# Kernel optimization log

Hardware: AMD Instinct MI355X
Metric: run time of the kernel (lower is better)

Reference implementation:

```python
import jax, jax.numpy as jnp
import numpy as np

B, N, S, C, H = 16, 64, 4096, 768, 8
HD = C // H
SCALE = HD ** -0.5
ASSIGN_EPS = 1.0


def hard_softmax(logits, axis):
    # softmax over `axis`, then straight-through one-hot argmax along `axis`
    y_soft = jax.nn.softmax(logits, axis=axis)
    idx = jnp.argmax(y_soft, axis=axis, keepdims=True)
    n = logits.shape[axis]
    shape = [1] * logits.ndim
    shape[axis] = n
    iota = jnp.arange(n).reshape(shape)
    y_hard = (iota == idx).astype(logits.dtype)
    return y_hard - jax.lax.stop_gradient(y_soft) + y_soft


def setup_inputs() -> dict:
    key = jax.random.key(0)
    ks = jax.random.split(key, 7)
    w = lambda k, shp: (jax.random.normal(k, shp, dtype=jnp.float32) * 0.02)
    return {
        'query': jax.random.normal(ks[0], (B, N, C), dtype=jnp.float32),
        'key_in': jax.random.normal(ks[1], (B, S, C), dtype=jnp.float32),
        'Wq': w(ks[2], (C, C)),
        'Wk': w(ks[3], (C, C)),
        'Wv': w(ks[4], (C, C)),
        'Wo': w(ks[5], (C, C)),
        'bo': jnp.zeros((C,), dtype=jnp.float32),
    }


def reference(query, key_in, Wq, Wk, Wv, Wo, bo):
    # linear projections (torch Linear: x @ W.T), split heads -> b h n d
    q = jnp.einsum('bnc,dc->bnd', query, Wq).reshape(B, N, H, HD).transpose(0, 2, 1, 3)
    k = jnp.einsum('bsc,dc->bsd', key_in, Wk).reshape(B, S, H, HD).transpose(0, 2, 1, 3)
    v = jnp.einsum('bsc,dc->bsd', key_in, Wv).reshape(B, S, H, HD).transpose(0, 2, 1, 3)
    raw_attn = jnp.einsum('bhnd,bhsd->bhns', q, k) * SCALE      # [B,H,N,S]
    attn = hard_softmax(raw_attn, axis=-2)                       # hard assign over groups N
    attn = attn / (attn.sum(axis=-1, keepdims=True) + ASSIGN_EPS)  # renorm over tokens S
    out = jnp.einsum('bhns,bhsd->bhnd', attn, v)                 # [B,H,N,HD]
    out = out.transpose(0, 2, 1, 3).reshape(B, N, C)
    out = jnp.einsum('bnc,dc->bnd', out, Wo) + bo
    return out
```

## Files before the change

### kernel.cpp

```cpp
#include <hip/hip_runtime.h>

#define BB 16
#define NN 64
#define SS 4096
#define CC 768
#define HH 8
#define HD 96

typedef __attribute__((ext_vector_type(8))) short bf16x8;
typedef __attribute__((ext_vector_type(4))) float f32x4;
typedef __attribute__((ext_vector_type(8))) unsigned short u16x8;

static __device__ __forceinline__ unsigned short f2bf(float x) {
  unsigned u = __float_as_uint(x);
  unsigned r = (u + 0x7fffu + ((u >> 16) & 1u)) >> 16;
  return (unsigned short)r;
}
static __device__ __forceinline__ float bf2f(unsigned short h) {
  return __uint_as_float(((unsigned)h) << 16);
}
static __device__ __forceinline__ void split2t(float f0, float f1,
                                               unsigned* hw, unsigned* lw) {
  unsigned u0 = __float_as_uint(f0), u1 = __float_as_uint(f1);
  *hw = (u0 >> 16) | (u1 & 0xffff0000u);
  float l0 = f0 - __uint_as_float(u0 & 0xffff0000u);
  float l1 = f1 - __uint_as_float(u1 & 0xffff0000u);
  unsigned v0 = __float_as_uint(l0), v1 = __float_as_uint(l1);
  *lw = (v0 >> 16) | (v1 & 0xffff0000u);
}

__global__ __launch_bounds__(256) void k_transpose(
    const float* __restrict__ src, float* __restrict__ dst) {
  __shared__ float tile[32][33];
  const int bx = blockIdx.x % 24, by = blockIdx.x / 24;
  const int tx = threadIdx.x & 31, ty = threadIdx.x >> 5;
#pragma unroll
  for (int k = 0; k < 4; ++k)
    tile[ty + k * 8][tx] = src[(size_t)(by * 32 + ty + k * 8) * CC + bx * 32 + tx];
  __syncthreads();
#pragma unroll
  for (int k = 0; k < 4; ++k)
    dst[(size_t)(bx * 32 + ty + k * 8) * CC + by * 32 + tx] = tile[tx][ty + k * 8];
}

__global__ __launch_bounds__(256) void k_q(
    const float* __restrict__ query, const float* __restrict__ WqT,
    double* __restrict__ q64g) {
  __shared__ double qin[2][CC];
  const int tid = threadIdx.x;
  const int rp = blockIdx.x / 3, cs = blockIdx.x % 3;
  const int r0 = rp * 2;

#pragma unroll
  for (int u = 0; u < 6; ++u) {
    int idx = tid + u * 256;
    int r = idx / CC, c = idx - r * CC;
    qin[r][c] = (double)query[(size_t)(r0 + r) * CC + c];
  }
  __syncthreads();

  const int j = cs * 256 + tid;
  double a0 = 0.0, a1 = 0.0;
  const float* wt = WqT + j;
  for (int e = 0; e < CC; ++e) {
    const double w = (double)wt[(size_t)e * CC];
    a0 += qin[0][e] * w;
    a1 += qin[1][e] * w;
  }
  q64g[(size_t)(r0 + 0) * CC + j] = a0;
  q64g[(size_t)(r0 + 1) * CC + j] = a1;
}

__global__ __launch_bounds__(256) void k_fold(
    const double* __restrict__ q64g, const float* __restrict__ Wk,
    double* __restrict__ qk64, unsigned short* __restrict__ qhp,
    unsigned short* __restrict__ qlp) {
  __shared__ double q64l[2][CC];
  const int tid = threadIdx.x;
  const int rp = blockIdx.x / 3, cs3 = blockIdx.x % 3;
  const int r0 = rp * 2;

#pragma unroll
  for (int u = 0; u < 6; ++u) {
    int idx = tid + u * 256;
    int r = idx / CC, c = idx - r * CC;
    q64l[r][c] = q64g[(size_t)(r0 + r) * CC + c];
  }
  __syncthreads();

  const int c = cs3 * 256 + tid;
  const double SC = 0.10206207261596575;
  const int csp = c >> 5, lkc = (c >> 3) & 3, jp = c & 7;

  for (int h = 0; h < HH; ++h) {
    double b0 = 0.0, b1 = 0.0;
    const float* wk = Wk + (size_t)(h * HD) * CC + c;
    const double* qh0 = &q64l[0][h * HD];
    const double* qh1 = &q64l[1][h * HD];
#pragma unroll 4
    for (int dd = 0; dd < HD; ++dd) {
      const double w = (double)wk[(size_t)dd * CC];
      b0 += qh0[dd] * w;
      b1 += qh1[dd] * w;
    }
    b0 *= SC; b1 *= SC;
    double av[2] = {b0, b1};
#pragma unroll
    for (int r = 0; r < 2; ++r) {
      const int row = r0 + r, b_ = row >> 6, n = row & 63;
      const int col512 = h * 64 + n;
      size_t o = ((size_t)(b_ * HH + h) * NN + n) * CC + c;
      qk64[o] = av[r];
      float f = (float)av[r];
      unsigned short hh16 = f2bf(f);
      size_t po = (((size_t)(b_ * 24 + csp) * 32 + (col512 >> 4)) * 64 +
                   (lkc * 16 + (col512 & 15))) * 8 + jp;
      qhp[po] = hh16;
      qlp[po] = f2bf(f - bf2f(hh16));
    }
  }
}

#define DELTA 1e-3f

__global__ __launch_bounds__(512) void k_filter_mfma(
    const float* __restrict__ key,
    const unsigned short* __restrict__ qhp, const unsigned short* __restrict__ qlp,
    unsigned char* __restrict__ assign_t, int* __restrict__ susp,
    int* __restrict__ scnt) {
  __shared__ unsigned short khi[2][64][72];
  __shared__ unsigned short klo[2][64][72];
  const int tid = threadIdx.x;
  const int lane = tid & 63;
  const int wn = tid >> 6;
  const int bid0 = blockIdx.x;
  const int swz = (bid0 & 7) * 128 + (bid0 >> 3);
  const int b = swz >> 6;
  const int s0 = (swz & 63) * 64;
  const int l16 = lane & 15;
  const int lk = lane >> 4;

  f32x4 acc[4][4];
#pragma unroll
  for (int m = 0; m < 4; ++m)
#pragma unroll
    for (int n = 0; n < 4; ++n) acc[m][n] = (f32x4){0.f, 0.f, 0.f, 0.f};

  const float* kbase = key + ((size_t)b * SS + s0) * CC;
  const int srow = tid >> 3, sc8 = tid & 7;

#define BBASE(cs) ((((size_t)(b * 24 + (cs)) * 32 + wn * 4) * 64 + lane) * 8)

  bf16x8 bhA[4], blA[4], bhB[4], blB[4];
  {
    float4 st0 = *(const float4*)(kbase + (size_t)srow * CC + sc8 * 8);
    float4 st1 = *(const float4*)(kbase + (size_t)srow * CC + sc8 * 8 + 4);
    union { u16x8 v; unsigned w[4]; } h8, l8;
    split2t(st0.x, st0.y, &h8.w[0], &l8.w[0]);
    split2t(st0.z, st0.w, &h8.w[1], &l8.w[1]);
    split2t(st1.x, st1.y, &h8.w[2], &l8.w[2]);
    split2t(st1.z, st1.w, &h8.w[3], &l8.w[3]);
    *(u16x8*)&khi[0][srow][sc8 * 8] = h8.v;
    *(u16x8*)&klo[0][srow][sc8 * 8] = l8.v;
    const size_t bb = BBASE(0);
#pragma unroll
    for (int n = 0; n < 4; ++n) {
      bhA[n] = *(const bf16x8*)(qhp + bb + (size_t)n * 512);
      blA[n] = *(const bf16x8*)(qlp + bb + (size_t)n * 512);
    }
  }
  __syncthreads();

  for (int t = 0; t < 12; ++t) {
    const int cur = t & 1;
    float4 st0, st1;
    if (t < 11) {
      const int cb = (t + 1) * 64;
      st0 = *(const float4*)(kbase + (size_t)srow * CC + cb + sc8 * 8);
      st1 = *(const float4*)(kbase + (size_t)srow * CC + cb + sc8 * 8 + 4);
    }
    {
      const int cs = t * 2;
      const size_t bbn = BBASE(cs + 1);
#pragma unroll
      for (int n = 0; n < 4; ++n) {
        bhB[n] = *(const bf16x8*)(qhp + bbn + (size_t)n * 512);
        blB[n] = *(const bf16x8*)(qlp + bbn + (size_t)n * 512);
      }
      bf16x8 ah[4], al_[4];
#pragma unroll
      for (int m = 0; m < 4; ++m) {
        ah[m]  = *(const bf16x8*)&khi[cur][m * 16 + l16][lk * 8];
        al_[m] = *(const bf16x8*)&klo[cur][m * 16 + l16][lk * 8];
      }
#pragma unroll
      for (int m = 0; m < 4; ++m)
#pragma unroll
        for (int n = 0; n < 4; ++n)
          acc[m][n] = __builtin_amdgcn_mfma_f32_16x16x32_bf16(ah[m], bhA[n], acc[m][n], 0, 0, 0);
#pragma unroll
      for (int m = 0; m < 4; ++m)
#pragma unroll
        for (int n = 0; n < 4; ++n)
          acc[m][n] = __builtin_amdgcn_mfma_f32_16x16x32_bf16(ah[m], blA[n], acc[m][n], 0, 0, 0);
#pragma unroll
      for (int m = 0; m < 4; ++m)
#pragma unroll
        for (int n = 0; n < 4; ++n)
          acc[m][n] = __builtin_amdgcn_mfma_f32_16x16x32_bf16(al_[m], bhA[n], acc[m][n], 0, 0, 0);
    }
    {
      if (t < 11) {
        const size_t bbn = BBASE(t * 2 + 2);
#pragma unroll
        for (int n = 0; n < 4; ++n) {
          bhA[n] = *(const bf16x8*)(qhp + bbn + (size_t)n * 512);
          blA[n] = *(const bf16x8*)(qlp + bbn + (size_t)n * 512);
        }
      }
      bf16x8 ah[4], al_[4];
#pragma unroll
      for (int m = 0; m < 4; ++m) {
        ah[m]  = *(const bf16x8*)&khi[cur][m * 16 + l16][32 + lk * 8];
        al_[m] = *(const bf16x8*)&klo[cur][m * 16 + l16][32 + lk * 8];
      }
#pragma unroll
      for (int m = 0; m < 4; ++m)
#pragma unroll
        for (int n = 0; n < 4; ++n)
          acc[m][n] = __builtin_amdgcn_mfma_f32_16x16x32_bf16(ah[m], bhB[n], acc[m][n], 0, 0, 0);
#pragma unroll
      for (int m = 0; m < 4; ++m)
#pragma unroll
        for (int n = 0; n < 4; ++n)
          acc[m][n] = __builtin_amdgcn_mfma_f32_16x16x32_bf16(ah[m], blB[n], acc[m][n], 0, 0, 0);
#pragma unroll
      for (int m = 0; m < 4; ++m)
#pragma unroll
        for (int n = 0; n < 4; ++n)
          acc[m][n] = __builtin_amdgcn_mfma_f32_16x16x32_bf16(al_[m], bhB[n], acc[m][n], 0, 0, 0);
    }

    if (t < 11) {
      union { u16x8 v; unsigned w[4]; } h8, l8;
      split2t(st0.x, st0.y, &h8.w[0], &l8.w[0]);
      split2t(st0.z, st0.w, &h8.w[1], &l8.w[1]);
      split2t(st1.x, st1.y, &h8.w[2], &l8.w[2]);
      split2t(st1.z, st1.w, &h8.w[3], &l8.w[3]);
      *(u16x8*)&khi[cur ^ 1][srow][sc8 * 8] = h8.v;
      *(u16x8*)&klo[cur ^ 1][srow][sc8 * 8] = l8.v;
    }
    __syncthreads();
  }
#undef BBASE

#pragma unroll
  for (int m = 0; m < 4; ++m) {
    const int tokbase = s0 + m * 16 + lk * 4;
#pragma unroll
    for (int r = 0; r < 4; ++r) {
      const int tok = tokbase + r;
      float m1 = -3.402823466e38f, m2 = -3.402823466e38f;
      int i1 = 0;
#pragma unroll
      for (int n = 0; n < 4; ++n) {
        float v = acc[m][n][r];
        int g = n * 16 + l16;
        if (v > m1) { m2 = m1; m1 = v; i1 = g; }
        else if (v > m2) m2 = v;
      }
#pragma unroll
      for (int off = 1; off <= 8; off <<= 1) {
        float om1 = __shfl_xor(m1, off);
        float om2 = __shfl_xor(m2, off);
        int oi1 = __shfl_xor(i1, off);
        if (om1 > m1 || (om1 == m1 && oi1 < i1)) {
          m2 = fmaxf(m1, fmaxf(m2, om2));
          m1 = om1; i1 = oi1;
        } else {
          m2 = fmaxf(om1, fmaxf(m2, om2));
        }
      }
      if (l16 == 0) {
        const int bh2 = b * 8 + wn;
        assign_t[((size_t)b * SS + tok) * 8 + wn] = (unsigned char)i1;
        if (m1 - m2 < DELTA) {
          int w = atomicAdd(&scnt[bh2], 1);
          susp[(size_t)bh2 * SS + w] = tok;
        }
      }
    }
  }
}

__global__ __launch_bounds__(256) void k_rescore(
    const float* __restrict__ key, const double* __restrict__ qk64,
    const int* __restrict__ susp, const int* __restrict__ scnt,
    unsigned char* __restrict__ assign_t) {
  __shared__ float krow[16][CC];
  __shared__ double l64[16][64];
  const int bh = blockIdx.x;
  const int cnt = scnt[bh];
  if (cnt == 0) return;
  const int b = bh >> 3, h = bh & 7;
  const int tid = threadIdx.x;
  const int n = tid >> 2, q = tid & 3;
  const double* qrow = qk64 + ((size_t)bh * NN + n) * CC + q * 192;

  for (int i0 = 0; i0 < cnt; i0 += 16) {
    const int nb = (cnt - i0 < 16) ? (cnt - i0) : 16;
    for (int r = 0; r < nb; ++r) {
      const int s = susp[(size_t)bh * SS + i0 + r];
      for (int u = tid; u < CC; u += 256)
        krow[r][u] = key[((size_t)b * SS + s) * CC + u];
    }
    __syncthreads();

    double acc[16];
#pragma unroll
    for (int r = 0; r < 16; ++r) acc[r] = 0.0;
    for (int c4 = 0; c4 < 48; ++c4) {
      const double w0 = qrow[c4 * 4 + 0];
      const double w1 = qrow[c4 * 4 + 1];
      const double w2 = qrow[c4 * 4 + 2];
      const double w3 = qrow[c4 * 4 + 3];
#pragma unroll
      for (int r = 0; r < 16; ++r) {
        float4 k4 = *(const float4*)&krow[r][q * 192 + c4 * 4];
        acc[r] += w0 * (double)k4.x;
        acc[r] += w1 * (double)k4.y;
        acc[r] += w2 * (double)k4.z;
        acc[r] += w3 * (double)k4.w;
      }
    }
#pragma unroll
    for (int r = 0; r < 16; ++r) {
      acc[r] += __shfl_xor(acc[r], 1);
      acc[r] += __shfl_xor(acc[r], 2);
    }
    if (q == 0) {
#pragma unroll
      for (int r = 0; r < 16; ++r) l64[r][n] = acc[r];
    }
    __syncthreads();
    if (tid < nb) {
      double best = l64[tid][0];
      int bi = 0;
      for (int n2 = 1; n2 < 64; ++n2)
        if (l64[tid][n2] > best) { best = l64[tid][n2]; bi = n2; }
      const int s = susp[(size_t)bh * SS + i0 + tid];
      assign_t[((size_t)b * SS + s) * 8 + h] = (unsigned char)bi;
    }
    __syncthreads();
  }
}

__global__ __launch_bounds__(256) void k_counts(
    const unsigned char* __restrict__ assign_t, int* __restrict__ counts) {
  __shared__ int hist[64];
  const int bh = blockIdx.x;
  const int b = bh >> 3, h = bh & 7;
  const int tid = threadIdx.x;
  if (tid < 64) hist[tid] = 0;
  __syncthreads();
  for (int s = tid; s < SS; s += 256)
    atomicAdd(&hist[assign_t[((size_t)b * SS + s) * 8 + h]], 1);
  __syncthreads();
  if (tid < 64) counts[bh * 64 + tid] = hist[tid];
}

__global__ __launch_bounds__(256) void k_convert(
    const float* __restrict__ keyhalf, unsigned short* __restrict__ kb16) {
  const int n8 = 8 * SS * CC / 8;
  int i = blockIdx.x * 256 + threadIdx.x;
  const int stride = gridDim.x * 256;
  for (; i < n8; i += stride) {
    float4 a = ((const float4*)keyhalf)[i * 2];
    float4 b = ((const float4*)keyhalf)[i * 2 + 1];
    u16x8 r;
    r[0] = f2bf(a.x); r[1] = f2bf(a.y); r[2] = f2bf(a.z); r[3] = f2bf(a.w);
    r[4] = f2bf(b.x); r[5] = f2bf(b.y); r[6] = f2bf(b.z); r[7] = f2bf(b.w);
    *(u16x8*)(kb16 + (size_t)i * 8) = r;
  }
}

__global__ __launch_bounds__(64) void k_rank(
    const unsigned char* __restrict__ assign_t, const int* __restrict__ counts,
    int* __restrict__ offsets, int* __restrict__ perm) {
  __shared__ int base[64];
  const int bh = blockIdx.x;
  const int b = bh >> 3, h = bh & 7;
  const int lane = threadIdx.x;

  int cn = counts[bh * 64 + lane];
  int off = cn;
#pragma unroll
  for (int d = 1; d < 64; d <<= 1) {
    int t = __shfl_up(off, d);
    if (lane >= d) off += t;
  }
  off -= cn;
  offsets[bh * 64 + lane] = off;
  base[lane] = off;

  for (int c = 0; c < SS / 64; ++c) {
    const int s = c * 64 + lane;
    const int g = (int)assign_t[((size_t)b * SS + s) * 8 + h];
    unsigned long long m = ~0ull;
#pragma unroll
    for (int k = 0; k < 6; ++k) {
      unsigned long long bk = __ballot((g >> k) & 1);
      m &= ((g >> k) & 1) ? bk : ~bk;
    }
    const int leader = __ffsll((unsigned long long)m) - 1;
    const int rankin = __popcll(m & ((1ull << lane) - 1ull));
    int baseo = 0;
    if (lane == leader) {
      baseo = base[g];
      base[g] = baseo + __popcll(m);
    }
    baseo = __shfl(baseo, leader);
    perm[(size_t)bh * SS + baseo + rankin] = s;
  }
}

__global__ __launch_bounds__(64) void k_gatherp(
    const unsigned short* __restrict__ kb16, const int* __restrict__ perm,
    const int* __restrict__ offsets, const int* __restrict__ counts,
    float* __restrict__ gsum, int b0) {
  const int bid = blockIdx.x;
  const int bl = bid >> 9;
  const int gbid = b0 * 512 + bid;
  const int bh = gbid >> 6;
  const int lane = threadIdx.x;

  const int off = offsets[gbid];
  const int cnt = counts[gbid];
  const int* pl = perm + (size_t)bh * SS + off;
  const unsigned short* kb = kb16 + (size_t)bl * SS * CC;

  float4 a0 = {0.f, 0.f, 0.f, 0.f}, b0v = a0, c0 = a0;
  int j = 0;
  for (; j + 3 < cnt; j += 4) {
    const int s0 = pl[j], s1 = pl[j + 1], s2 = pl[j + 2], s3 = pl[j + 3];
    const ushort4* k0 = (const ushort4*)(kb + (size_t)s0 * CC);
    const ushort4* k1 = (const ushort4*)(kb + (size_t)s1 * CC);
    const ushort4* k2 = (const ushort4*)(kb + (size_t)s2 * CC);
    const ushort4* k3 = (const ushort4*)(kb + (size_t)s3 * CC);
    ushort4 x0 = k0[lane], x1 = k0[lane + 64], x2 = k0[lane + 128];
    ushort4 y0 = k1[lane], y1 = k1[lane + 64], y2 = k1[lane + 128];
    ushort4 z0 = k2[lane], z1 = k2[lane + 64], z2 = k2[lane + 128];
    ushort4 w0 = k3[lane], w1 = k3[lane + 64], w2 = k3[lane + 128];
    a0.x += bf2f(x0.x); a0.y += bf2f(x0.y); a0.z += bf2f(x0.z); a0.w += bf2f(x0.w);
    b0v.x += bf2f(x1.x); b0v.y += bf2f(x1.y); b0v.z += bf2f(x1.z); b0v.w += bf2f(x1.w);
    c0.x += bf2f(x2.x); c0.y += bf2f(x2.y); c0.z += bf2f(x2.z); c0.w += bf2f(x2.w);
    a0.x += bf2f(y0.x); a0.y += bf2f(y0.y); a0.z += bf2f(y0.z); a0.w += bf2f(y0.w);
    b0v.x += bf2f(y1.x); b0v.y += bf2f(y1.y); b0v.z += bf2f(y1.z); b0v.w += bf2f(y1.w);
    c0.x += bf2f(y2.x); c0.y += bf2f(y2.y); c0.z += bf2f(y2.z); c0.w += bf2f(y2.w);
    a0.x += bf2f(z0.x); a0.y += bf2f(z0.y); a0.z += bf2f(z0.z); a0.w += bf2f(z0.w);
    b0v.x += bf2f(z1.x); b0v.y += bf2f(z1.y); b0v.z += bf2f(z1.z); b0v.w += bf2f(z1.w);
    c0.x += bf2f(z2.x); c0.y += bf2f(z2.y); c0.z += bf2f(z2.z); c0.w += bf2f(z2.w);
    a0.x += bf2f(w0.x); a0.y += bf2f(w0.y); a0.z += bf2f(w0.z); a0.w += bf2f(w0.w);
    b0v.x += bf2f(w1.x); b0v.y += bf2f(w1.y); b0v.z += bf2f(w1.z); b0v.w += bf2f(w1.w);
    c0.x += bf2f(w2.x); c0.y += bf2f(w2.y); c0.z += bf2f(w2.z); c0.w += bf2f(w2.w);
  }
  for (; j < cnt; ++j) {
    const int s0 = pl[j];
    const ushort4* k0 = (const ushort4*)(kb + (size_t)s0 * CC);
    ushort4 x0 = k0[lane], x1 = k0[lane + 64], x2 = k0[lane + 128];
    a0.x += bf2f(x0.x); a0.y += bf2f(x0.y); a0.z += bf2f(x0.z); a0.w += bf2f(x0.w);
    b0v.x += bf2f(x1.x); b0v.y += bf2f(x1.y); b0v.z += bf2f(x1.z); b0v.w += bf2f(x1.w);
    c0.x += bf2f(x2.x); c0.y += bf2f(x2.y); c0.z += bf2f(x2.z); c0.w += bf2f(x2.w);
  }
  float4* go = (float4*)(gsum + (size_t)gbid * CC);
  go[lane] = a0; go[lane + 64] = b0v; go[lane + 128] = c0;
}

__global__ __launch_bounds__(256) void k_v(
    const float* __restrict__ gsum, const int* __restrict__ counts,
    const float* __restrict__ WvT, float* __restrict__ vrg) {
  __shared__ float gs[2][HH][CC];
  const int tid = threadIdx.x;
  const int rp = blockIdx.x / 3, cs = blockIdx.x % 3;
  const int r0 = rp * 2;

  for (int r = 0; r < 2; ++r) {
    int row = r0 + r, b = row >> 6, n = row & 63;
    for (int h = 0; h < HH; ++h) {
      const float sc = 1.f / (float)(counts[(b * HH + h) * NN + n] + 1);
      const float* src = gsum + ((size_t)(b * HH + h) * NN + n) * CC;
      for (int m = 0; m < 3; ++m)
        gs[r][h][tid + m * 256] = src[tid + m * 256] * sc;
    }
  }
  __syncthreads();

  const int j = cs * 256 + tid;
  const int hj = j / HD;
  float a0 = 0.f, a1 = 0.f;
  const float* wt = WvT + j;
  for (int e4 = 0; e4 < CC / 4; ++e4) {
    const int e = e4 * 4;
    float4 g0 = *(const float4*)&gs[0][hj][e];
    float4 g1 = *(const float4*)&gs[1][hj][e];
    const float w0 = wt[(size_t)e * CC];
    const float w1 = wt[(size_t)(e + 1) * CC];
    const float w2 = wt[(size_t)(e + 2) * CC];
    const float w3 = wt[(size_t)(e + 3) * CC];
    a0 = fmaf(g0.x, w0, a0); a0 = fmaf(g0.y, w1, a0);
    a0 = fmaf(g0.z, w2, a0); a0 = fmaf(g0.w, w3, a0);
    a1 = fmaf(g1.x, w0, a1); a1 = fmaf(g1.y, w1, a1);
    a1 = fmaf(g1.z, w2, a1); a1 = fmaf(g1.w, w3, a1);
  }
  vrg[(size_t)(r0 + 0) * CC + j] = a0;
  vrg[(size_t)(r0 + 1) * CC + j] = a1;
}

__global__ __launch_bounds__(256) void k_o(
    const float* __restrict__ vrg, const float* __restrict__ WoT,
    const float* __restrict__ bo, float* __restrict__ out) {
  __shared__ float vr[2][CC];
  const int tid = threadIdx.x;
  const int rp = blockIdx.x / 3, cs = blockIdx.x % 3;
  const int r0 = rp * 2;

#pragma unroll
  for (int u = 0; u < 6; ++u) {
    int idx = tid + u * 256;
    int r = idx / CC, c = idx - r * CC;
    vr[r][c] = vrg[(size_t)(r0 + r) * CC + c];
  }
  __syncthreads();

  const int j = cs * 256 + tid;
  float a0 = bo[j], a1 = a0;
  const float* wt = WoT + j;
  for (int e4 = 0; e4 < CC / 4; ++e4) {
    const int e = e4 * 4;
    float4 v0 = *(const float4*)&vr[0][e];
    float4 v1 = *(const float4*)&vr[1][e];
    const float w0 = wt[(size_t)e * CC];
    const float w1 = wt[(size_t)(e + 1) * CC];
    const float w2 = wt[(size_t)(e + 2) * CC];
    const float w3 = wt[(size_t)(e + 3) * CC];
    a0 = fmaf(v0.x, w0, a0); a0 = fmaf(v0.y, w1, a0);
    a0 = fmaf(v0.z, w2, a0); a0 = fmaf(v0.w, w3, a0);
    a1 = fmaf(v1.x, w0, a1); a1 = fmaf(v1.y, w1, a1);
    a1 = fmaf(v1.z, w2, a1); a1 = fmaf(v1.w, w3, a1);
  }
  out[(size_t)(r0 + 0) * CC + j] = a0;
  out[(size_t)(r0 + 1) * CC + j] = a1;
}

extern "C" void kernel_launch(void* const* d_in, const int* in_sizes, int n_in,
                              void* d_out, int out_size, void* d_ws, size_t ws_size,
                              hipStream_t stream) {
  const float* query = (const float*)d_in[0];
  const float* key   = (const float*)d_in[1];
  const float* Wq    = (const float*)d_in[2];
  const float* Wk    = (const float*)d_in[3];
  const float* Wv    = (const float*)d_in[4];
  const float* Wo    = (const float*)d_in[5];
  const float* bo    = (const float*)d_in[6];
  float* out = (float*)d_out;

  char* ws = (char*)d_ws;
  double* qk64           = (double*)(ws);
  unsigned short* kb16   = (unsigned short*)(ws);
  unsigned short* qhp    = (unsigned short*)(ws + 50331648);
  unsigned short* qlp    = (unsigned short*)(ws + 62914560);
  float* gsum            = (float*)(ws + 50331648);
  unsigned char* assign_t= (unsigned char*)(ws + 75497472);
  int* susp              = (int*)(ws + 76021760);
  int* scnt              = (int*)(ws + 78118912);
  int* counts            = (int*)(ws + 78119424);
  int* offsets           = (int*)(ws + 78152192);
  int* perm              = (int*)(ws + 78184960);
  float* WqT             = (float*)(ws + 80282112);
  float* WvT             = (float*)(ws + 82641408);
  float* WoT             = (float*)(ws + 85000704);
  double* q64g           = (double*)(ws + 87360000);
  float* vrg             = (float*)(ws + 93651456);

  hipMemsetAsync(scnt, 0, 512, stream);
  k_transpose<<<576, 256, 0, stream>>>(Wq, WqT);
  k_transpose<<<576, 256, 0, stream>>>(Wv, WvT);
  k_transpose<<<576, 256, 0, stream>>>(Wo, WoT);
  k_q<<<1536, 256, 0, stream>>>(query, WqT, q64g);
  k_fold<<<1536, 256, 0, stream>>>(q64g, Wk, qk64, qhp, qlp);
  k_filter_mfma<<<1024, 512, 0, stream>>>(key, qhp, qlp, assign_t, susp, scnt);
  k_rescore<<<128, 256, 0, stream>>>(key, qk64, susp, scnt, assign_t);
  k_counts<<<128, 256, 0, stream>>>(assign_t, counts);
  k_rank<<<128, 64, 0, stream>>>(assign_t, counts, offsets, perm);
  k_convert<<<1024, 256, 0, stream>>>(key, kb16);
  k_gatherp<<<4096, 64, 0, stream>>>(kb16, perm, offsets, counts, gsum, 0);
  k_convert<<<1024, 256, 0, stream>>>(key + (size_t)8 * SS * CC, kb16);
  k_gatherp<<<4096, 64, 0, stream>>>(kb16, perm, offsets, counts, gsum, 8);
  k_v<<<1536, 256, 0, stream>>>(gsum, counts, WvT, vrg);
  k_o<<<1536, 256, 0, stream>>>(vrg, WoT, bo, out);
}
```

Before: 803.2 us.

## Double the filter kernel's token tile to 128 rows per block

The MFMA filter kernel now handles 128 key tokens per block instead of 64, halving the grid to 512 blocks. Each block loads the query-fold B fragments (qhp/qlp) once and reuses them across twice as many M tiles, which cuts redundant global reads of those operands. The cost is twice the LDS per block, twice the accumulator registers (acc 8x4), and fewer blocks, which may lower occupancy and latency hiding. The key staging is also restructured so each thread loads 16 floats.

```diff
diff --git a/kernel.cpp b/kernel.cpp
--- a/kernel.cpp
+++ b/kernel.cpp
@@ -128,40 +128,78 @@
     const unsigned short* __restrict__ qhp, const unsigned short* __restrict__ qlp,
     unsigned char* __restrict__ assign_t, int* __restrict__ susp,
     int* __restrict__ scnt) {
-  __shared__ unsigned short khi[2][64][72];
-  __shared__ unsigned short klo[2][64][72];
+  __shared__ unsigned short khi[2][128][72];
+  __shared__ unsigned short klo[2][128][72];
   const int tid = threadIdx.x;
   const int lane = tid & 63;
   const int wn = tid >> 6;
   const int bid0 = blockIdx.x;
-  const int swz = (bid0 & 7) * 128 + (bid0 >> 3);
-  const int b = swz >> 6;
-  const int s0 = (swz & 63) * 64;
+  const int swz = (bid0 & 7) * 64 + (bid0 >> 3);
+  const int b = swz >> 5;
+  const int s0 = (swz & 31) * 128;
   const int l16 = lane & 15;
   const int lk = lane >> 4;
 
-  f32x4 acc[4][4];
-#pragma unroll
-  for (int m = 0; m < 4; ++m)
+  f32x4 acc[8][4];
+#pragma unroll
+  for (int m = 0; m < 8; ++m)
 #pragma unroll
     for (int n = 0; n < 4; ++n) acc[m][n] = (f32x4){0.f, 0.f, 0.f, 0.f};
 
   const float* kbase = key + ((size_t)b * SS + s0) * CC;
-  const int srow = tid >> 3, sc8 = tid & 7;
+  const int srow = tid >> 2, c16 = (tid & 3) * 16;
 
 #define BBASE(cs) ((((size_t)(b * 24 + (cs)) * 32 + wn * 4) * 64 + lane) * 8)
+#define STAGE(buf, cb)                                                         \
+  {                                                                            \
+    const float* sp = kbase + (size_t)srow * CC + (cb) + c16;                  \
+    float4 x0 = *(const float4*)(sp);                                          \
+    float4 x1 = *(const float4*)(sp + 4);                                      \
+    float4 x2 = *(const float4*)(sp + 8);                                      \
+    float4 x3 = *(const float4*)(sp + 12);                                     \
+    union { u16x8 v; unsigned w[4]; } ha, la, hb, lb;                          \
+    split2t(x0.x, x0.y, &ha.w[0], &la.w[0]);                                   \
+    split2t(x0.z, x0.w, &ha.w[1], &la.w[1]);                                   \
+    split2t(x1.x, x1.y, &ha.w[2], &la.w[2]);                                   \
+    split2t(x1.z, x1.w, &ha.w[3], &la.w[3]);                                   \
+    split2t(x2.x, x2.y, &hb.w[0], &lb.w[0]);                                   \
+    split2t(x2.z, x2.w, &hb.w[1], &lb.w[1]);                                   \
+    split2t(x3.x, x3.y, &hb.w[2], &lb.w[2]);                                   \
+    split2t(x3.z, x3.w, &hb.w[3], &lb.w[3]);                                   \
+    *(u16x8*)&khi[buf][srow][c16] = ha.v;                                      \
+    *(u16x8*)&khi[buf][srow][c16 + 8] = hb.v;                                  \
+    *(u16x8*)&klo[buf][srow][c16] = la.v;                                      \
+    *(u16x8*)&klo[buf][srow][c16 + 8] = lb.v;                                  \
+  }
+
+#define MHALF(m0, coloff, BH, BL)                                              \
+  {                                                                            \
+    bf16x8 ah[4], al_[4];                                                      \
+    _Pragma("unroll")                                                          \
+    for (int mm = 0; mm < 4; ++mm) {                                           \
+      ah[mm]  = *(const bf16x8*)&khi[cur][(m0 + mm) * 16 + l16][coloff + lk * 8]; \
+      al_[mm] = *(const bf16x8*)&klo[cur][(m0 + mm) * 16 + l16][coloff + lk * 8]; \
+    }                                                                          \
+    _Pragma("unroll")                                                          \
+    for (int mm = 0; mm < 4; ++mm)                                             \
+      _Pragma("unroll")                                                        \
+      for (int n = 0; n < 4; ++n)                                              \
+        acc[m0 + mm][n] = __builtin_amdgcn_mfma_f32_16x16x32_bf16(ah[mm], BH[n], acc[m0 + mm][n], 0, 0, 0); \
+    _Pragma("unroll")                                                          \
+    for (int mm = 0; mm < 4; ++mm)                                             \
+      _Pragma("unroll")                                                        \
+      for (int n = 0; n < 4; ++n)                                              \
+        acc[m0 + mm][n] = __builtin_amdgcn_mfma_f32_16x16x32_bf16(ah[mm], BL[n], acc[m0 + mm][n], 0, 0, 0); \
+    _Pragma("unroll")                                                          \
+    for (int mm = 0; mm < 4; ++mm)                                             \
+      _Pragma("unroll")                                                        \
+      for (int n = 0; n < 4; ++n)                                              \
+        acc[m0 + mm][n] = __builtin_amdgcn_mfma_f32_16x16x32_bf16(al_[mm], BH[n], acc[m0 + mm][n], 0, 0, 0); \
+  }
 
   bf16x8 bhA[4], blA[4], bhB[4], blB[4];
   {
-    float4 st0 = *(const float4*)(kbase + (size_t)srow * CC + sc8 * 8);
-    float4 st1 = *(const float4*)(kbase + (size_t)srow * CC + sc8 * 8 + 4);
-    union { u16x8 v; unsigned w[4]; } h8, l8;
-    split2t(st0.x, st0.y, &h8.w[0], &l8.w[0]);
-    split2t(st0.z, st0.w, &h8.w[1], &l8.w[1]);
-    split2t(st1.x, st1.y, &h8.w[2], &l8.w[2]);
-    split2t(st1.z, st1.w, &h8.w[3], &l8.w[3]);
-    *(u16x8*)&khi[0][srow][sc8 * 8] = h8.v;
-    *(u16x8*)&klo[0][srow][sc8 * 8] = l8.v;
+    STAGE(0, 0);
     const size_t bb = BBASE(0);
 #pragma unroll
     for (int n = 0; n < 4; ++n) {
@@ -173,41 +211,15 @@
 
   for (int t = 0; t < 12; ++t) {
     const int cur = t & 1;
-    float4 st0, st1;
-    if (t < 11) {
-      const int cb = (t + 1) * 64;
-      st0 = *(const float4*)(kbase + (size_t)srow * CC + cb + sc8 * 8);
-      st1 = *(const float4*)(kbase + (size_t)srow * CC + cb + sc8 * 8 + 4);
-    }
     {
-      const int cs = t * 2;
-      const size_t bbn = BBASE(cs + 1);
+      const size_t bbn = BBASE(t * 2 + 1);
 #pragma unroll
       for (int n = 0; n < 4; ++n) {
         bhB[n] = *(const bf16x8*)(qhp + bbn + (size_t)n * 512);
         blB[n] = *(const bf16x8*)(qlp + bbn + (size_t)n * 512);
       }
-      bf16x8 ah[4], al_[4];
-#pragma unroll
-      for (int m = 0; m < 4; ++m) {
-        ah[m]  = *(const bf16x8*)&khi[cur][m * 16 + l16][lk * 8];
-        al_[m] = *(const bf16x8*)&klo[cur][m * 16 + l16][lk * 8];
-      }
-#pragma unroll
-      for (int m = 0; m < 4; ++m)
-#pragma unroll
-        for (int n = 0; n < 4; ++n)
-          acc[m][n] = __builtin_amdgcn_mfma_f32_16x16x32_bf16(ah[m], bhA[n], acc[m][n], 0, 0, 0);
-#pragma unroll
-      for (int m = 0; m < 4; ++m)
-#pragma unroll
-        for (int n = 0; n < 4; ++n)
-          acc[m][n] = __builtin_amdgcn_mfma_f32_16x16x32_bf16(ah[m], blA[n], acc[m][n], 0, 0, 0);
-#pragma unroll
-      for (int m = 0; m < 4; ++m)
-#pragma unroll
-        for (int n = 0; n < 4; ++n)
-          acc[m][n] = __builtin_amdgcn_mfma_f32_16x16x32_bf16(al_[m], bhA[n], acc[m][n], 0, 0, 0);
+      MHALF(0, 0, bhA, blA);
+      MHALF(4, 0, bhA, blA);
     }
     {
       if (t < 11) {
@@ -218,44 +230,21 @@
           blA[n] = *(const bf16x8*)(qlp + bbn + (size_t)n * 512);
         }
       }
-      bf16x8 ah[4], al_[4];
-#pragma unroll
-      for (int m = 0; m < 4; ++m) {
-        ah[m]  = *(const bf16x8*)&khi[cur][m * 16 + l16][32 + lk * 8];
-        al_[m] = *(const bf16x8*)&klo[cur][m * 16 + l16][32 + lk * 8];
-      }
-#pragma unroll
-      for (int m = 0; m < 4; ++m)
-#pragma unroll
-        for (int n = 0; n < 4; ++n)
-          acc[m][n] = __builtin_amdgcn_mfma_f32_16x16x32_bf16(ah[m], bhB[n], acc[m][n], 0, 0, 0);
-#pragma unroll
-      for (int m = 0; m < 4; ++m)
-#pragma unroll
-        for (int n = 0; n < 4; ++n)
-          acc[m][n] = __builtin_amdgcn_mfma_f32_16x16x32_bf16(ah[m], blB[n], acc[m][n], 0, 0, 0);
-#pragma unroll
-      for (int m = 0; m < 4; ++m)
-#pragma unroll
-        for (int n = 0; n < 4; ++n)
-          acc[m][n] = __builtin_amdgcn_mfma_f32_16x16x32_bf16(al_[m], bhB[n], acc[m][n], 0, 0, 0);
+      MHALF(0, 32, bhB, blB);
+      MHALF(4, 32, bhB, blB);
     }
 
     if (t < 11) {
-      union { u16x8 v; unsigned w[4]; } h8, l8;
-      split2t(st0.x, st0.y, &h8.w[0], &l8.w[0]);
-      split2t(st0.z, st0.w, &h8.w[1], &l8.w[1]);
-      split2t(st1.x, st1.y, &h8.w[2], &l8.w[2]);
-      split2t(st1.z, st1.w, &h8.w[3], &l8.w[3]);
-      *(u16x8*)&khi[cur ^ 1][srow][sc8 * 8] = h8.v;
-      *(u16x8*)&klo[cur ^ 1][srow][sc8 * 8] = l8.v;
+      STAGE(cur ^ 1, (t + 1) * 64);
     }
     __syncthreads();
   }
+#undef MHALF
+#undef STAGE
 #undef BBASE
 
 #pragma unroll
-  for (int m = 0; m < 4; ++m) {
+  for (int m = 0; m < 8; ++m) {
     const int tokbase = s0 + m * 16 + lk * 4;
 #pragma unroll
     for (int r = 0; r < 4; ++r) {
@@ -588,7 +577,7 @@
   k_transpose<<<576, 256, 0, stream>>>(Wo, WoT);
   k_q<<<1536, 256, 0, stream>>>(query, WqT, q64g);
   k_fold<<<1536, 256, 0, stream>>>(q64g, Wk, qk64, qhp, qlp);
-  k_filter_mfma<<<1024, 512, 0, stream>>>(key, qhp, qlp, assign_t, susp, scnt);
+  k_filter_mfma<<<512, 512, 0, stream>>>(key, qhp, qlp, assign_t, susp, scnt);
   k_rescore<<<128, 256, 0, stream>>>(key, qk64, susp, scnt, assign_t);
   k_counts<<<128, 256, 0, stream>>>(assign_t, counts);
   k_rank<<<128, 64, 0, stream>>>(assign_t, counts, offsets, perm);
```

After: 795.3 us. About the same (-1.0%).
